# Optimization experiments

Hardware: AMD Instinct MI355X
Metric: run time of the kernel (lower is better)

The kernel has to match this reference:

```python
import jax, jax.numpy as jnp
import numpy as np

D = 1024      # model_dim
H = 16        # num_heads
HD = D // H   # head_size
B = 4
S = 2048


def setup_inputs() -> dict:
    key = jax.random.key(0)
    ks = jax.random.split(key, 6)
    sc = 1.0 / np.sqrt(D)
    embedded = jax.random.normal(ks[0], (B, S, D), dtype=jnp.float32)
    # Per-head projection weights stacked: [H, D, HD] (nn.Linear, bias=False)
    Wq = jax.random.normal(ks[1], (H, D, HD), dtype=jnp.float32) * sc
    Wk = jax.random.normal(ks[2], (H, D, HD), dtype=jnp.float32) * sc
    Wv = jax.random.normal(ks[3], (H, D, HD), dtype=jnp.float32) * sc
    # Output projection nn.Linear(D, D) with bias
    Wo = jax.random.normal(ks[4], (D, D), dtype=jnp.float32) * sc
    bo = jax.random.normal(ks[5], (D,), dtype=jnp.float32) * sc
    return {"embedded": embedded, "Wq": Wq, "Wk": Wk, "Wv": Wv, "Wo": Wo, "bo": bo}


def reference(embedded, Wq, Wk, Wv, Wo, bo):
    # q,k,v: [B, H, S, HD]
    q = jnp.einsum('bsd,hde->bhse', embedded, Wq)
    k = jnp.einsum('bsd,hde->bhse', embedded, Wk)
    v = jnp.einsum('bsd,hde->bhse', embedded, Wv)
    scores = jnp.einsum('bhse,bhte->bhst', q, k) / jnp.sqrt(jnp.float32(HD))
    causal = jnp.tril(jnp.ones((S, S), dtype=bool))  # [S, S]
    scores = jnp.where(causal, scores, -jnp.inf)
    attn = jax.nn.softmax(scores, axis=-1)
    ctx = jnp.einsum('bhst,bhte->bhse', attn, v)  # [B, H, S, HD]
    # concat heads -> [B, S, D]
    concat = jnp.transpose(ctx, (0, 2, 1, 3)).reshape(B, S, D)
    # dropout=0.0 -> identity
    return concat @ Wo.T + bo
```

## Files before the change

kernel.cpp:

```cpp
#include <hip/hip_runtime.h>
#include <hip/hip_bf16.h>
#include <stdint.h>
#include <stddef.h>

typedef __bf16 bf16;
typedef __bf16 bf16x8 __attribute__((ext_vector_type(8)));
typedef float f32x4 __attribute__((ext_vector_type(4)));
typedef float f32x16 __attribute__((ext_vector_type(16)));


__device__ __forceinline__ void gload16(const void* g, void* lds) {
  __builtin_amdgcn_global_load_lds(
      (const __attribute__((address_space(1))) unsigned int*)(uintptr_t)g,
      (__attribute__((address_space(3))) unsigned int*)(unsigned int)(uintptr_t)lds,
      16, 0, 0);
}

__device__ __forceinline__ bf16x8 lds_read8(const bf16* base, int row, int slot) {
  const char* p = (const char*)base + row * 128 + ((slot ^ (row & 7)) << 4);
  return *(const bf16x8*)p;
}

__device__ __forceinline__ float f3max(float a, float b, float c) {
  return fmaxf(fmaxf(a, b), c);
}


__global__ void k_cvt_embed(const float* __restrict__ src, bf16* __restrict__ dst) {
  int i = blockIdx.x * blockDim.x + threadIdx.x;
  const float4* s4 = (const float4*)src;
  float4 a = s4[2 * i], b = s4[2 * i + 1];
  bf16x8 v;
  v[0] = (bf16)a.x; v[1] = (bf16)a.y; v[2] = (bf16)a.z; v[3] = (bf16)a.w;
  v[4] = (bf16)b.x; v[5] = (bf16)b.y; v[6] = (bf16)b.z; v[7] = (bf16)b.w;
  ((bf16x8*)dst)[i] = v;
}


__global__ void k_cvt_w(const float* __restrict__ Wq, const float* __restrict__ Wk,
                        const float* __restrict__ Wv, const float* __restrict__ Wo,
                        bf16* __restrict__ WT, bf16* __restrict__ WoB) {
  int i = blockIdx.x * blockDim.x + threadIdx.x;
  if (i < 16 * 192 * 1024) {
    int h = i / (192 * 1024);
    int rem = i - h * (192 * 1024);
    int r = rem >> 10;
    int d = rem & 1023;
    const float* W = (r < 64) ? Wq : (r < 128 ? Wk : Wv);
    int e = r & 63;
    WT[i] = (bf16)W[h * 65536 + d * 64 + e];
  } else {
    int j = i - 16 * 192 * 1024;
    WoB[j] = (bf16)Wo[j];
  }
}


__launch_bounds__(256, 2)
__global__ void k_qkv(const bf16* __restrict__ E, const bf16* __restrict__ WT,
                      bf16* __restrict__ Qo, bf16* __restrict__ Ko, bf16* __restrict__ Vo) {
  __shared__ __align__(16) bf16 As[128 * 64];
  __shared__ __align__(16) bf16 Bs[192 * 64];
  const int h = blockIdx.y;
  const int m0 = blockIdx.x * 128;
  const int tid = threadIdx.x;
  const int w = tid >> 6, lane = tid & 63;
  const int wm = w >> 1, wn = w & 1;
  const int cl = lane & 15, g4 = lane >> 4;
  const int srow = lane >> 3;
  const int scol = ((lane & 7) ^ (lane >> 3)) << 3;
  const bf16* Wh = WT + (size_t)h * 192 * 1024;
  f32x4 zero = {0.f, 0.f, 0.f, 0.f};
  f32x4 acc[4][6];
#pragma unroll
  for (int m = 0; m < 4; ++m)
#pragma unroll
    for (int n = 0; n < 6; ++n) acc[m][n] = zero;

  for (int kt = 0; kt < 16; ++kt) {
    const int k0 = kt * 64;
    __syncthreads();
#pragma unroll
    for (int c = 0; c < 4; ++c) {
      int cc = w * 4 + c;
      gload16(E + (size_t)(m0 + cc * 8 + srow) * 1024 + k0 + scol, (char*)As + cc * 1024);
    }
#pragma unroll
    for (int c = 0; c < 6; ++c) {
      int cc = w * 6 + c;
      gload16(Wh + (size_t)(cc * 8 + srow) * 1024 + k0 + scol, (char*)Bs + cc * 1024);
    }
    __syncthreads();
#pragma unroll
    for (int kk = 0; kk < 2; ++kk) {
      bf16x8 a[4], b[6];
#pragma unroll
      for (int m = 0; m < 4; ++m) a[m] = lds_read8(As, wm * 64 + m * 16 + cl, kk * 4 + g4);
#pragma unroll
      for (int n = 0; n < 6; ++n) b[n] = lds_read8(Bs, wn * 96 + n * 16 + cl, kk * 4 + g4);
#pragma unroll
      for (int m = 0; m < 4; ++m)
#pragma unroll
        for (int n = 0; n < 6; ++n)
          acc[m][n] = __builtin_amdgcn_mfma_f32_16x16x32_bf16(a[m], b[n], acc[m][n], 0, 0, 0);
    }
  }
#pragma unroll
  for (int n = 0; n < 6; ++n) {
    int ncol = wn * 96 + n * 16 + cl;
    int which = ncol >> 6, e = ncol & 63;
    bf16* dst = which == 0 ? Qo : (which == 1 ? Ko : Vo);
    const float sc = (which == 0) ? 0.18033688f : 1.0f;
#pragma unroll
    for (int m = 0; m < 4; ++m) {
#pragma unroll
      for (int r = 0; r < 4; ++r) {
        int row = m0 + wm * 64 + m * 16 + g4 * 4 + r;
        int bb = row >> 11, ss = row & 2047;
        dst[(((size_t)(bb * 16 + h) * 2048 + ss) << 6) + e] = (bf16)(acc[m][n][r] * sc);
      }
    }
  }
}


__launch_bounds__(512)
__global__ void k_attn(const bf16* __restrict__ Qg, const bf16* __restrict__ Kg,
                       const bf16* __restrict__ Vg, bf16* __restrict__ CTX) {
  __shared__ __align__(16) bf16 KS[2][8192];
  __shared__ __align__(16) bf16 VT[2][2][4096];
  const int b = blockIdx.x;
  const int bh = b & 63;
  const int g = b >> 6;
  const int qt = (g < 4) ? g : 11 - g;
  const int q0 = qt * 256;
  const int tid = threadIdx.x, w = tid >> 6, lane = tid & 63;
  const int ql = lane & 31, hi = lane >> 5;
  const int q = q0 + 32 * w + ql;
  const int qmin = q0 + 32 * w;
  const int qmax = qmin + 31;
  const bf16* Qb = Qg + (size_t)bh * (2048 * 64);
  const bf16* Kb = Kg + (size_t)bh * (2048 * 64);
  const bf16* Vb = Vg + (size_t)bh * (2048 * 64);
  const int ntk = 2 * qt + 2;

  bf16x8 qf[4];
#pragma unroll
  for (int ks = 0; ks < 4; ++ks)
    qf[ks] = *(const bf16x8*)(Qb + (size_t)q * 64 + ks * 16 + hi * 8);

  f32x16 o0, o1;
#pragma unroll
  for (int i = 0; i < 16; ++i) { o0[i] = 0.f; o1[i] = 0.f; }
  float mr = -1e30f, ls = 0.f;

  const int srowK = w * 8 + (lane >> 3);
  const int scolK = ((lane & 7) ^ ((lane >> 3) & 7)) << 3;
  const int lanep = (lane & ~12) | ((lane & 4) << 1) | ((lane & 8) >> 1);
  int offs[4];
#pragma unroll
  for (int ks = 0; ks < 4; ++ks) offs[ks] = (ks * 32 + hi * 16) ^ ((ql & 7) << 4);

  auto do_half = [&](int kv0h, const char* kbase, const char* vbase) {
    f32x16 s0, s1;
#pragma unroll
    for (int i = 0; i < 16; ++i) { s0[i] = 0.f; s1[i] = 0.f; }
    __builtin_amdgcn_s_setprio(1);
#pragma unroll
    for (int ks = 0; ks < 4; ++ks) {
      bf16x8 k0 = *(const bf16x8*)(kbase + ql * 128 + offs[ks]);
      bf16x8 k1 = *(const bf16x8*)(kbase + (32 + ql) * 128 + offs[ks]);
      s0 = __builtin_amdgcn_mfma_f32_32x32x16_bf16(k0, qf[ks], s0, 0, 0, 0);
      s1 = __builtin_amdgcn_mfma_f32_32x32x16_bf16(k1, qf[ks], s1, 0, 0, 0);
    }
    __builtin_amdgcn_s_setprio(0);
    if (kv0h + 63 > qmin) {
      int dqh = q - kv0h - 4 * hi;
#pragma unroll
      for (int r = 0; r < 16; ++r) {
        const int c = (r & 3) + 8 * (r >> 2);
        if (c > dqh) s0[r] = -1e30f;
        if (c + 32 > dqh) s1[r] = -1e30f;
      }
    }
    float x0 = f3max(s0[0], s0[1], s0[2]);
    float x1 = f3max(s0[3], s0[4], s0[5]);
    float x2 = f3max(s0[6], s0[7], s0[8]);
    float x3 = f3max(s0[9], s0[10], s0[11]);
    float x4 = f3max(s0[12], s0[13], s0[14]);
    float x5 = f3max(s0[15], s1[0], s1[1]);
    float x6 = f3max(s1[2], s1[3], s1[4]);
    float x7 = f3max(s1[5], s1[6], s1[7]);
    float x8 = f3max(s1[8], s1[9], s1[10]);
    float x9 = f3max(s1[11], s1[12], s1[13]);
    float xa = fmaxf(s1[14], s1[15]);
    float y0 = f3max(x0, x1, x2);
    float y1 = f3max(x3, x4, x5);
    float y2 = f3max(x6, x7, x8);
    float y3 = fmaxf(x9, xa);
    float pmax = f3max(y0, y1, fmaxf(y2, y3));
    pmax = fmaxf(pmax, __shfl_xor(pmax, 32));
    if (__any(pmax - mr > 8.0f)) {
      float mnew = fmaxf(mr, pmax);
      float al = exp2f(mr - mnew);
      mr = mnew; ls *= al;
#pragma unroll
      for (int i = 0; i < 16; ++i) { o0[i] *= al; o1[i] *= al; }
    }
#pragma unroll
    for (int i = 0; i < 16; ++i) {
      s0[i] = exp2f(s0[i] - mr);
      s1[i] = exp2f(s1[i] - mr);
    }
    float a8[8];
#pragma unroll
    for (int i = 0; i < 8; ++i) a8[i] = (s0[i] + s0[i + 8]) + (s1[i] + s1[i + 8]);
    float rs = ((a8[0] + a8[1]) + (a8[2] + a8[3])) + ((a8[4] + a8[5]) + (a8[6] + a8[7]));
    rs += __shfl_xor(rs, 32);
    ls += rs;
    bf16x8 pf[4];
#pragma unroll
    for (int j = 0; j < 8; ++j) {
      pf[0][j] = (bf16)s0[j];
      pf[1][j] = (bf16)s0[8 + j];
      pf[2][j] = (bf16)s1[j];
      pf[3][j] = (bf16)s1[8 + j];
    }
    __builtin_amdgcn_s_setprio(1);
#pragma unroll
    for (int ks = 0; ks < 4; ++ks) {
      bf16x8 v0 = *(const bf16x8*)(vbase + ql * 128 + offs[ks]);
      bf16x8 v1 = *(const bf16x8*)(vbase + (32 + ql) * 128 + offs[ks]);
      o0 = __builtin_amdgcn_mfma_f32_32x32x16_bf16(v0, pf[ks], o0, 0, 0, 0);
      o1 = __builtin_amdgcn_mfma_f32_32x32x16_bf16(v1, pf[ks], o1, 0, 0, 0);
    }
    __builtin_amdgcn_s_setprio(0);
  };

  {
    gload16(Kb + (size_t)srowK * 64 + scolK, (char*)KS[0] + w * 1024);
    gload16(Kb + (size_t)(64 + srowK) * 64 + scolK, (char*)KS[0] + 8192 + w * 1024);
    bf16x8 v0 = *(const bf16x8*)(Vb + (size_t)lane * 64 + w * 8);
    bf16x8 v1 = *(const bf16x8*)(Vb + (size_t)(64 + lane) * 64 + w * 8);
#pragma unroll
    for (int j = 0; j < 8; ++j) {
      *(bf16*)((char*)VT[0][0] + w * 1024 + j * 128 + ((lanep * 2) ^ (j << 4))) = v0[j];
      *(bf16*)((char*)VT[0][1] + w * 1024 + j * 128 + ((lanep * 2) ^ (j << 4))) = v1[j];
    }
  }

  int cur = 0;
  for (int t = 0; t < ntk; ++t) {
    const int kv0 = t * 128;
    __syncthreads();
    bf16x8 vn0, vn1;
    const bool more = (t + 1 < ntk);
    if (more) {
      const int kn = kv0 + 128;
      vn0 = *(const bf16x8*)(Vb + (size_t)(kn + lane) * 64 + w * 8);
      vn1 = *(const bf16x8*)(Vb + (size_t)(kn + 64 + lane) * 64 + w * 8);
      gload16(Kb + (size_t)(kn + srowK) * 64 + scolK, (char*)KS[cur ^ 1] + w * 1024);
      gload16(Kb + (size_t)(kn + 64 + srowK) * 64 + scolK, (char*)KS[cur ^ 1] + 8192 + w * 1024);
    }
    if (kv0 <= qmax)
      do_half(kv0, (const char*)KS[cur], (const char*)VT[cur][0]);
    if (more) {
#pragma unroll
      for (int j = 0; j < 8; ++j) {
        *(bf16*)((char*)VT[cur ^ 1][0] + w * 1024 + j * 128 + ((lanep * 2) ^ (j << 4))) = vn0[j];
        *(bf16*)((char*)VT[cur ^ 1][1] + w * 1024 + j * 128 + ((lanep * 2) ^ (j << 4))) = vn1[j];
      }
    }
    if (kv0 + 64 <= qmax)
      do_half(kv0 + 64, (const char*)KS[cur] + 8192, (const char*)VT[cur][1]);
    cur ^= 1;
  }

  const float inv = 1.0f / ls;
  const int bb = bh >> 4, hh = bh & 15;
  bf16* Cp = CTX + ((size_t)(bb * 2048 + q) * 1024) + hh * 64;
#pragma unroll
  for (int r = 0; r < 16; ++r) {
    int d0 = (r & 3) + 8 * (r >> 2) + 4 * hi;
    Cp[d0] = (bf16)(o0[r] * inv);
    Cp[32 + d0] = (bf16)(o1[r] * inv);
  }
}


__launch_bounds__(256, 2)
__global__ void k_oproj(const bf16* __restrict__ X, const bf16* __restrict__ Wb,
                        const float* __restrict__ bo, float* __restrict__ out) {
  __shared__ __align__(16) bf16 As[128 * 64];
  __shared__ __align__(16) bf16 Bs[128 * 64];
  const int m0 = blockIdx.x * 128, n0 = blockIdx.y * 128;
  const int tid = threadIdx.x, w = tid >> 6, lane = tid & 63;
  const int wm = w >> 1, wn = w & 1;
  const int cl = lane & 15, g4 = lane >> 4;
  const int srow = lane >> 3;
  const int scol = ((lane & 7) ^ (lane >> 3)) << 3;
  f32x4 zero = {0.f, 0.f, 0.f, 0.f};
  f32x4 acc[4][4];
#pragma unroll
  for (int m = 0; m < 4; ++m)
#pragma unroll
    for (int n = 0; n < 4; ++n) acc[m][n] = zero;

  for (int kt = 0; kt < 16; ++kt) {
    const int k0 = kt * 64;
    __syncthreads();
#pragma unroll
    for (int c = 0; c < 4; ++c) {
      int cc = w * 4 + c;
      gload16(X + (size_t)(m0 + cc * 8 + srow) * 1024 + k0 + scol, (char*)As + cc * 1024);
      gload16(Wb + (size_t)(n0 + cc * 8 + srow) * 1024 + k0 + scol, (char*)Bs + cc * 1024);
    }
    __syncthreads();
#pragma unroll
    for (int kk = 0; kk < 2; ++kk) {
      bf16x8 a[4], b[4];
#pragma unroll
      for (int m = 0; m < 4; ++m) a[m] = lds_read8(As, wm * 64 + m * 16 + cl, kk * 4 + g4);
#pragma unroll
      for (int n = 0; n < 4; ++n) b[n] = lds_read8(Bs, wn * 64 + n * 16 + cl, kk * 4 + g4);
#pragma unroll
      for (int m = 0; m < 4; ++m)
#pragma unroll
        for (int n = 0; n < 4; ++n)
          acc[m][n] = __builtin_amdgcn_mfma_f32_16x16x32_bf16(a[m], b[n], acc[m][n], 0, 0, 0);
    }
  }
#pragma unroll
  for (int n = 0; n < 4; ++n) {
    int col = n0 + wn * 64 + n * 16 + cl;
    float bias = bo[col];
#pragma unroll
    for (int m = 0; m < 4; ++m)
#pragma unroll
      for (int r = 0; r < 4; ++r) {
        int row = m0 + wm * 64 + m * 16 + g4 * 4 + r;
        out[(size_t)row * 1024 + col] = acc[m][n][r] + bias;
      }
  }
}


extern "C" void kernel_launch(void* const* d_in, const int* in_sizes, int n_in,
                              void* d_out, int out_size, void* d_ws, size_t ws_size,
                              hipStream_t stream) {
  const float* emb = (const float*)d_in[0];
  const float* Wq  = (const float*)d_in[1];
  const float* Wk  = (const float*)d_in[2];
  const float* Wv  = (const float*)d_in[3];
  const float* Wo  = (const float*)d_in[4];
  const float* bo  = (const float*)d_in[5];
  float* out = (float*)d_out;

  const size_t NEED = (size_t)72 << 20;
  if (ws_size < NEED) return;

  char* ws = (char*)d_ws;
  bf16* E   = (bf16*)(ws);
  bf16* WT  = (bf16*)(ws + ((size_t)16 << 20));
  bf16* WoB = (bf16*)(ws + ((size_t)22 << 20));
  bf16* Qw  = (bf16*)(ws + ((size_t)24 << 20));
  bf16* Kw  = (bf16*)(ws + ((size_t)40 << 20));
  bf16* Vw  = (bf16*)(ws + ((size_t)56 << 20));
  bf16* CTX = E;

  k_cvt_embed<<<4096, 256, 0, stream>>>(emb, E);
  k_cvt_w<<<16384, 256, 0, stream>>>(Wq, Wk, Wv, Wo, WT, WoB);
  k_qkv<<<dim3(64, 16), 256, 0, stream>>>(E, WT, Qw, Kw, Vw);
  k_attn<<<512, 512, 0, stream>>>(Qw, Kw, Vw, CTX);
  k_oproj<<<dim3(64, 8), 256, 0, stream>>>(CTX, WoB, bo, out);
}
```

Measured before the change: 180.0 us.

## Write V transposed from QKV kernel and stage it into LDS with async loads

The QKV projection kernel now stores V in a per-head transposed [dim, seq] layout with 4-wide vector stores. The attention kernel can then stage V tiles into LDS with direct global-to-LDS loads instead of register loads followed by scalar transposing LDS writes. K rows are loaded under a permuted row order, and the causal mask index math changes to match the new score layout. This removes per-element LDS scatter and register staging in the attention loop, at the cost of strided writes in the projection epilogue and a more fragile index mapping.

```diff
diff --git a/kernel.cpp b/kernel.cpp
--- a/kernel.cpp
+++ b/kernel.cpp
@@ -4,6 +4,7 @@
 #include <stddef.h>
 
 typedef __bf16 bf16;
+typedef __bf16 bf16x4 __attribute__((ext_vector_type(4)));
 typedef __bf16 bf16x8 __attribute__((ext_vector_type(8)));
 typedef float f32x4 __attribute__((ext_vector_type(4)));
 typedef float f32x16 __attribute__((ext_vector_type(16)));
@@ -58,7 +59,7 @@
 
 __launch_bounds__(256, 2)
 __global__ void k_qkv(const bf16* __restrict__ E, const bf16* __restrict__ WT,
-                      bf16* __restrict__ Qo, bf16* __restrict__ Ko, bf16* __restrict__ Vo) {
+                      bf16* __restrict__ Qo, bf16* __restrict__ Ko, bf16* __restrict__ Vt) {
   __shared__ __align__(16) bf16 As[128 * 64];
   __shared__ __align__(16) bf16 Bs[192 * 64];
   const int h = blockIdx.y;
@@ -109,15 +110,27 @@
   for (int n = 0; n < 6; ++n) {
     int ncol = wn * 96 + n * 16 + cl;
     int which = ncol >> 6, e = ncol & 63;
-    bf16* dst = which == 0 ? Qo : (which == 1 ? Ko : Vo);
-    const float sc = (which == 0) ? 0.18033688f : 1.0f;
-#pragma unroll
-    for (int m = 0; m < 4; ++m) {
-#pragma unroll
-      for (int r = 0; r < 4; ++r) {
-        int row = m0 + wm * 64 + m * 16 + g4 * 4 + r;
+    if (which == 2) {
+#pragma unroll
+      for (int m = 0; m < 4; ++m) {
+        int row = m0 + wm * 64 + m * 16 + g4 * 4;
         int bb = row >> 11, ss = row & 2047;
-        dst[(((size_t)(bb * 16 + h) * 2048 + ss) << 6) + e] = (bf16)(acc[m][n][r] * sc);
+        bf16x4 vv;
+#pragma unroll
+        for (int r = 0; r < 4; ++r) vv[r] = (bf16)acc[m][n][r];
+        *(bf16x4*)(Vt + ((size_t)(bb * 16 + h) * 64 + e) * 2048 + ss) = vv;
+      }
+    } else {
+      bf16* dst = (which == 0) ? Qo : Ko;
+      const float sc = (which == 0) ? 0.18033688f : 1.0f;
+#pragma unroll
+      for (int m = 0; m < 4; ++m) {
+#pragma unroll
+        for (int r = 0; r < 4; ++r) {
+          int row = m0 + wm * 64 + m * 16 + g4 * 4 + r;
+          int bb = row >> 11, ss = row & 2047;
+          dst[(((size_t)(bb * 16 + h) * 2048 + ss) << 6) + e] = (bf16)(acc[m][n][r] * sc);
+        }
       }
     }
   }
@@ -126,9 +139,9 @@
 
 __launch_bounds__(512)
 __global__ void k_attn(const bf16* __restrict__ Qg, const bf16* __restrict__ Kg,
-                       const bf16* __restrict__ Vg, bf16* __restrict__ CTX) {
+                       const bf16* __restrict__ Vtg, bf16* __restrict__ CTX) {
   __shared__ __align__(16) bf16 KS[2][8192];
-  __shared__ __align__(16) bf16 VT[2][2][4096];
+  __shared__ __align__(16) bf16 VT[2][8192];
   const int b = blockIdx.x;
   const int bh = b & 63;
   const int g = b >> 6;
@@ -141,7 +154,7 @@
   const int qmax = qmin + 31;
   const bf16* Qb = Qg + (size_t)bh * (2048 * 64);
   const bf16* Kb = Kg + (size_t)bh * (2048 * 64);
-  const bf16* Vb = Vg + (size_t)bh * (2048 * 64);
+  const bf16* Vb = Vtg + (size_t)bh * (64 * 2048);
   const int ntk = 2 * qt + 2;
 
   bf16x8 qf[4];
@@ -155,13 +168,24 @@
   float mr = -1e30f, ls = 0.f;
 
   const int srowK = w * 8 + (lane >> 3);
+  const int phiRow = (srowK & ~12) | ((srowK & 4) << 1) | ((srowK & 8) >> 1);
   const int scolK = ((lane & 7) ^ ((lane >> 3) & 7)) << 3;
-  const int lanep = (lane & ~12) | ((lane & 4) << 1) | ((lane & 8) >> 1);
+  const int vrow0 = w * 4 + (lane >> 4);
+  const int vkey0 = ((lane & 15) ^ (vrow0 & 7)) * 8;
+  const int vrow1 = 32 + vrow0;
+  const int vkey1 = ((lane & 15) ^ (vrow1 & 7)) * 8;
   int offs[4];
 #pragma unroll
   for (int ks = 0; ks < 4; ++ks) offs[ks] = (ks * 32 + hi * 16) ^ ((ql & 7) << 4);
 
-  auto do_half = [&](int kv0h, const char* kbase, const char* vbase) {
+  auto stage = [&](int kv, int buf) {
+    gload16(Kb + (size_t)(kv + phiRow) * 64 + scolK, (char*)KS[buf] + w * 1024);
+    gload16(Kb + (size_t)(kv + 64 + phiRow) * 64 + scolK, (char*)KS[buf] + 8192 + w * 1024);
+    gload16(Vb + (size_t)vrow0 * 2048 + kv + vkey0, (char*)VT[buf] + w * 1024);
+    gload16(Vb + (size_t)vrow1 * 2048 + kv + vkey1, (char*)VT[buf] + 8192 + w * 1024);
+  };
+
+  auto do_half = [&](int kv0h, const char* kbase, const char* vtb, int halfB) {
     f32x16 s0, s1;
 #pragma unroll
     for (int i = 0; i < 16; ++i) { s0[i] = 0.f; s1[i] = 0.f; }
@@ -175,12 +199,12 @@
     }
     __builtin_amdgcn_s_setprio(0);
     if (kv0h + 63 > qmin) {
-      int dqh = q - kv0h - 4 * hi;
+      int dqh = q - kv0h - 8 * hi;
 #pragma unroll
       for (int r = 0; r < 16; ++r) {
-        const int c = (r & 3) + 8 * (r >> 2);
-        if (c > dqh) s0[r] = -1e30f;
-        if (c + 32 > dqh) s1[r] = -1e30f;
+        const int c0 = (r & 7) + ((r & 8) << 1);
+        if (c0 > dqh) s0[r] = -1e30f;
+        if (c0 + 32 > dqh) s1[r] = -1e30f;
       }
     }
     float x0 = f3max(s0[0], s0[1], s0[2]);
@@ -229,50 +253,25 @@
     __builtin_amdgcn_s_setprio(1);
 #pragma unroll
     for (int ks = 0; ks < 4; ++ks) {
-      bf16x8 v0 = *(const bf16x8*)(vbase + ql * 128 + offs[ks]);
-      bf16x8 v1 = *(const bf16x8*)(vbase + (32 + ql) * 128 + offs[ks]);
+      bf16x8 v0 = *(const bf16x8*)(vtb + ql * 256 + halfB + offs[ks]);
+      bf16x8 v1 = *(const bf16x8*)(vtb + (32 + ql) * 256 + halfB + offs[ks]);
       o0 = __builtin_amdgcn_mfma_f32_32x32x16_bf16(v0, pf[ks], o0, 0, 0, 0);
       o1 = __builtin_amdgcn_mfma_f32_32x32x16_bf16(v1, pf[ks], o1, 0, 0, 0);
     }
     __builtin_amdgcn_s_setprio(0);
   };
 
-  {
-    gload16(Kb + (size_t)srowK * 64 + scolK, (char*)KS[0] + w * 1024);
-    gload16(Kb + (size_t)(64 + srowK) * 64 + scolK, (char*)KS[0] + 8192 + w * 1024);
-    bf16x8 v0 = *(const bf16x8*)(Vb + (size_t)lane * 64 + w * 8);
-    bf16x8 v1 = *(const bf16x8*)(Vb + (size_t)(64 + lane) * 64 + w * 8);
-#pragma unroll
-    for (int j = 0; j < 8; ++j) {
-      *(bf16*)((char*)VT[0][0] + w * 1024 + j * 128 + ((lanep * 2) ^ (j << 4))) = v0[j];
-      *(bf16*)((char*)VT[0][1] + w * 1024 + j * 128 + ((lanep * 2) ^ (j << 4))) = v1[j];
-    }
-  }
+  stage(0, 0);
 
   int cur = 0;
   for (int t = 0; t < ntk; ++t) {
     const int kv0 = t * 128;
     __syncthreads();
-    bf16x8 vn0, vn1;
-    const bool more = (t + 1 < ntk);
-    if (more) {
-      const int kn = kv0 + 128;
-      vn0 = *(const bf16x8*)(Vb + (size_t)(kn + lane) * 64 + w * 8);
-      vn1 = *(const bf16x8*)(Vb + (size_t)(kn + 64 + lane) * 64 + w * 8);
-      gload16(Kb + (size_t)(kn + srowK) * 64 + scolK, (char*)KS[cur ^ 1] + w * 1024);
-      gload16(Kb + (size_t)(kn + 64 + srowK) * 64 + scolK, (char*)KS[cur ^ 1] + 8192 + w * 1024);
-    }
+    if (t + 1 < ntk) stage(kv0 + 128, cur ^ 1);
     if (kv0 <= qmax)
-      do_half(kv0, (const char*)KS[cur], (const char*)VT[cur][0]);
-    if (more) {
-#pragma unroll
-      for (int j = 0; j < 8; ++j) {
-        *(bf16*)((char*)VT[cur ^ 1][0] + w * 1024 + j * 128 + ((lanep * 2) ^ (j << 4))) = vn0[j];
-        *(bf16*)((char*)VT[cur ^ 1][1] + w * 1024 + j * 128 + ((lanep * 2) ^ (j << 4))) = vn1[j];
-      }
-    }
+      do_half(kv0, (const char*)KS[cur], (const char*)VT[cur], 0);
     if (kv0 + 64 <= qmax)
-      do_half(kv0 + 64, (const char*)KS[cur] + 8192, (const char*)VT[cur][1]);
+      do_half(kv0 + 64, (const char*)KS[cur] + 8192, (const char*)VT[cur], 128);
     cur ^= 1;
   }
 
@@ -365,12 +364,12 @@
   bf16* WoB = (bf16*)(ws + ((size_t)22 << 20));
   bf16* Qw  = (bf16*)(ws + ((size_t)24 << 20));
   bf16* Kw  = (bf16*)(ws + ((size_t)40 << 20));
-  bf16* Vw  = (bf16*)(ws + ((size_t)56 << 20));
+  bf16* Vtw = (bf16*)(ws + ((size_t)56 << 20));
   bf16* CTX = E;
 
   k_cvt_embed<<<4096, 256, 0, stream>>>(emb, E);
   k_cvt_w<<<16384, 256, 0, stream>>>(Wq, Wk, Wv, Wo, WT, WoB);
-  k_qkv<<<dim3(64, 16), 256, 0, stream>>>(E, WT, Qw, Kw, Vw);
-  k_attn<<<512, 512, 0, stream>>>(Qw, Kw, Vw, CTX);
+  k_qkv<<<dim3(64, 16), 256, 0, stream>>>(E, WT, Qw, Kw, Vtw);
+  k_attn<<<512, 512, 0, stream>>>(Qw, Kw, Vtw, CTX);
   k_oproj<<<dim3(64, 8), 256, 0, stream>>>(CTX, WoB, bo, out);
 }
```

Result: faster. 170.6 us (-5.2%).
